# Performance work log

Measured on AMD Instinct MI355X. Metric: run time of the kernel, lower is better.

Reference implementation:

```python
import jax, jax.numpy as jnp
import numpy as np

S, B, D = 2048, 2, 2048      # seq, batch, hidden  (x is [S, B, D])
H, KV, HD = 16, 4, 128        # n_head, n_kv_head, head_dim
N_REP = H // KV               # GQA repeat factor
THETA = 10000.0


def setup_inputs() -> dict:
    key = jax.random.key(0)
    ks = jax.random.split(key, 5)
    sc = 1.0 / np.sqrt(D)
    x = jax.random.normal(ks[0], (S, B, D), jnp.float32)
    Wq = jax.random.normal(ks[1], (D, H * HD), jnp.float32) * sc
    Wk = jax.random.normal(ks[2], (D, KV * HD), jnp.float32) * sc
    Wv = jax.random.normal(ks[3], (D, KV * HD), jnp.float32) * sc
    Wo = jax.random.normal(ks[4], (H * HD, D), jnp.float32) * sc
    return {"x": x, "Wq": Wq, "Wk": Wk, "Wv": Wv, "Wo": Wo}


def _rope_cos_sin(seq_len, dim, theta):
    inv_freq = 1.0 / (theta ** (jnp.arange(0, dim, 2, dtype=jnp.float32) / dim))
    t = jnp.arange(seq_len, dtype=jnp.float32)
    freqs = jnp.outer(t, inv_freq)                  # [S, dim/2]
    emb = jnp.concatenate([freqs, freqs], axis=-1)  # [S, dim]
    return jnp.cos(emb), jnp.sin(emb)


def _rotate_half(u):
    u1, u2 = jnp.split(u, 2, axis=-1)
    return jnp.concatenate([-u2, u1], axis=-1)


def reference(x, Wq, Wk, Wv, Wo):
    # projections (torch Linear without bias; W stored as [in, out] here)
    q = (x @ Wq).reshape(S, B, H, HD)
    k = (x @ Wk).reshape(S, B, KV, HD)
    v = (x @ Wv).reshape(S, B, KV, HD)

    # RoPE (full rotary, partial_rotary_factor == 1.0)
    cos, sin = _rope_cos_sin(S, HD, THETA)
    cos = cos[:, None, None, :]  # [S,1,1,HD] broadcasts over B, heads
    sin = sin[:, None, None, :]
    q = q * cos + _rotate_half(q) * sin
    k = k * cos + _rotate_half(k) * sin

    # GQA: repeat_interleave kv heads to match query heads
    k = jnp.repeat(k, N_REP, axis=2)
    v = jnp.repeat(v, N_REP, axis=2)

    # [S,B,H,HD] -> [B,H,S,HD]
    q = q.transpose(1, 2, 0, 3)
    k = k.transpose(1, 2, 0, 3)
    v = v.transpose(1, 2, 0, 3)

    # causal SDPA (dropout_p = 0 in eval)
    scale = 1.0 / np.sqrt(HD)
    scores = jnp.einsum('bhqd,bhkd->bhqk', q, k) * scale
    causal = jnp.tril(jnp.ones((S, S), dtype=bool))
    scores = jnp.where(causal, scores, jnp.finfo(scores.dtype).min)
    probs = jax.nn.softmax(scores, axis=-1)
    out = jnp.einsum('bhqk,bhkd->bhqd', probs, v)

    # [B,H,S,HD] -> [S,B,D], then output projection
    out = out.transpose(2, 0, 1, 3).reshape(S, B, D)
    return out @ Wo
```

## Files before the change

### kernel.cpp

```cpp
#include <hip/hip_runtime.h>
#include <hip/hip_bf16.h>
#include <cstdint>
#include <math.h>

#define S_LEN   2048
#define B_SZ    2
#define D_MODEL 2048
#define NH      16
#define NKV     4
#define HD      128
#define ROWS    (S_LEN * B_SZ)
#define NQKV    3072
#define SCALE   0.08838834764831845f

typedef __attribute__((ext_vector_type(8))) short short8;
typedef __attribute__((ext_vector_type(4))) float f32x4;

__device__ __forceinline__ short f2bf(float f) {
  union { float f; unsigned u; } v; v.f = f;
  unsigned r = v.u + 0x7fffu + ((v.u >> 16) & 1u);
  return (short)(r >> 16);
}
__device__ __forceinline__ float bf2f(short x) {
  union { unsigned u; float f; } v;
  v.u = ((unsigned)(unsigned short)x) << 16;
  return v.f;
}

__device__ __forceinline__ void async16(const short* g, short* l) {
  __builtin_amdgcn_global_load_lds(
      (const __attribute__((address_space(1))) void*)(uintptr_t)(const void*)g,
      (__attribute__((address_space(3))) void*)(uintptr_t)(void*)l,
      16, 0, 0);
}

__global__ void cvt_bf16_kernel(const float* __restrict__ src, short* __restrict__ dst, int n4) {
  int t = blockIdx.x * blockDim.x + threadIdx.x;
  if (t >= n4) return;
  float4 v = ((const float4*)src)[t];
  short4 o;
  o.x = f2bf(v.x); o.y = f2bf(v.y); o.z = f2bf(v.z); o.w = f2bf(v.w);
  *(short4*)(dst + (size_t)t * 4) = o;
}

__global__ void wtrans_qkv_kernel(const float* __restrict__ Wq,
                                  const float* __restrict__ Wk,
                                  const float* __restrict__ Wv,
                                  short* __restrict__ dst) {
  __shared__ float tile[32][33];
  const int bx = blockIdx.x;
  const float* src;
  int Ndim, n0, drow;
  if (bx < 64)      { src = Wq; Ndim = 2048; n0 = bx * 32;        drow = n0; }
  else if (bx < 80) { src = Wk; Ndim = 512;  n0 = (bx - 64) * 32; drow = 2048 + n0; }
  else              { src = Wv; Ndim = 512;  n0 = (bx - 80) * 32; drow = 2560 + n0; }
  const int k0 = blockIdx.y * 32;
  for (int r = threadIdx.y; r < 32; r += 8)
    tile[r][threadIdx.x] = src[(size_t)(k0 + r) * Ndim + n0 + threadIdx.x];
  __syncthreads();
  for (int r = threadIdx.y; r < 32; r += 8)
    dst[(size_t)(drow + r) * 2048 + k0 + threadIdx.x] = f2bf(tile[threadIdx.x][r]);
}

__global__ void wtrans_kernel(const float* __restrict__ src, short* __restrict__ dst,
                              int Kdim, int Ndim) {
  __shared__ float tile[32][33];
  int n0 = blockIdx.x * 32, k0 = blockIdx.y * 32;
  for (int r = threadIdx.y; r < 32; r += 8)
    tile[r][threadIdx.x] = src[(size_t)(k0 + r) * Ndim + n0 + threadIdx.x];
  __syncthreads();
  for (int r = threadIdx.y; r < 32; r += 8)
    dst[(size_t)(n0 + r) * Kdim + k0 + threadIdx.x] = f2bf(tile[threadIdx.x][r]);
}

template<int BM, int BF16OUT>
__global__ __launch_bounds__(512, 2) void gemm2_kernel(const short* __restrict__ A,
    const short* __restrict__ Bt, void* __restrict__ Cv, int N, int K) {
  constexpr int MI  = BM / 32;
  constexpr int PH  = MI / 4;
  constexpr int APW = BM / 128;
  constexpr int TC  = APW + 2;
  constexpr int ASZ = BM * 32;
  constexpr int BSZ = 256 * 32;
  constexpr int BUFS = ASZ + BSZ;
  __shared__ alignas(16) short lds[4 * BUFS];

  const int tid  = threadIdx.x;
  const int w    = tid >> 6, lane = tid & 63;
  const int quad = lane >> 4, lr = lane & 15;
  const int wm   = w >> 2, wn = w & 3;

  const int nwg = gridDim.x;
  const int id  = (blockIdx.x & 7) * (nwg >> 3) + (blockIdx.x >> 3);
  const int nbx = N >> 8;
  const int bx = id % nbx, by = id / nbx;
  const int m0 = by * BM, n0 = bx * 256;

  const short* gA = A  + (size_t)(m0 + w * (16 * APW) + (lane >> 2)) * K + (lane & 3) * 8;
  const short* gB = Bt + (size_t)(n0 + w * 32 + (lane >> 2)) * K + (lane & 3) * 8;

  const int aoff = (wm * (BM / 2) + lr) * 32 + quad * 8;
  const int boff = (wn * 64 + lr) * 32 + quad * 8;

  f32x4 acc[MI][4];
#pragma unroll
  for (int i = 0; i < MI; ++i)
#pragma unroll
    for (int j = 0; j < 4; ++j) acc[i][j] = (f32x4){0.f, 0.f, 0.f, 0.f};

  auto stageA = [&](int t) {
    short* la = lds + (t & 3) * BUFS;
    const short* g = gA + t * 32;
#pragma unroll
    for (int c = 0; c < APW; ++c)
      async16(g + (size_t)c * 16 * K, la + (w * APW + c) * 512);
  };
  auto stageB = [&](int t) {
    short* lb = lds + (t & 3) * BUFS + ASZ;
    const short* g = gB + t * 32;
#pragma unroll
    for (int c = 0; c < 2; ++c)
      async16(g + (size_t)c * 16 * K, lb + (w * 2 + c) * 512);
  };

  const int NT = K >> 5;
  stageA(0); stageB(0); stageA(1); stageB(1); stageA(2); stageB(2);
  asm volatile("s_waitcnt vmcnt(%0)" :: "n"(2 * TC) : "memory");
  __builtin_amdgcn_s_barrier();

  for (int t = 0; t < NT; ++t) {
    const short* la = lds + (t & 3) * BUFS;
    const short* lb = la + ASZ;
    const bool pre = (t + 3) < NT;

    short8 a0[4], b0[4];
#pragma unroll
    for (int j = 0; j < 4; ++j) b0[j] = *(const short8*)(lb + boff + j * 512);
#pragma unroll
    for (int i = 0; i < 4; ++i) a0[i] = *(const short8*)(la + aoff + i * 512);
    if (pre) stageA(t + 3);
    if (PH == 1 && pre) stageB(t + 3);
    __builtin_amdgcn_s_barrier();
    __builtin_amdgcn_s_setprio(1);
#pragma unroll
    for (int i = 0; i < 4; ++i)
#pragma unroll
      for (int j = 0; j < 4; ++j)
        acc[i][j] = __builtin_amdgcn_mfma_f32_16x16x32_bf16(a0[i], b0[j], acc[i][j], 0, 0, 0);
    __builtin_amdgcn_s_setprio(0);

    if (PH == 2) {
      __builtin_amdgcn_s_barrier();
      short8 a1[4];
#pragma unroll
      for (int i = 0; i < 4; ++i) a1[i] = *(const short8*)(la + aoff + (4 + i) * 512);
      if (pre) stageB(t + 3);
      __builtin_amdgcn_s_barrier();
      __builtin_amdgcn_s_setprio(1);
#pragma unroll
      for (int i = 0; i < 4; ++i)
#pragma unroll
        for (int j = 0; j < 4; ++j)
          acc[4 + i][j] = __builtin_amdgcn_mfma_f32_16x16x32_bf16(a1[i], b0[j], acc[4 + i][j], 0, 0, 0);
      __builtin_amdgcn_s_setprio(0);
    }

    if (t < NT - 1) {
      if (t < NT - 3)       asm volatile("s_waitcnt vmcnt(%0)" :: "n"(2 * TC) : "memory");
      else if (t == NT - 3) asm volatile("s_waitcnt vmcnt(%0)" :: "n"(TC) : "memory");
      else                  asm volatile("s_waitcnt vmcnt(0)" ::: "memory");
      __builtin_amdgcn_s_barrier();
    }
  }

#pragma unroll
  for (int i = 0; i < MI; ++i) {
    const int row = m0 + wm * (BM / 2) + i * 16 + quad * 4;
#pragma unroll
    for (int j = 0; j < 4; ++j) {
      const int col = n0 + wn * 64 + j * 16 + lr;
#pragma unroll
      for (int r = 0; r < 4; ++r) {
        const float v = acc[i][j][r];
        if (BF16OUT) ((short*)Cv)[(size_t)(row + r) * N + col] = f2bf(v);
        else         ((float*)Cv)[(size_t)(row + r) * N + col] = v;
      }
    }
  }
}

__global__ void rope_kernel(const short* __restrict__ QKVb, short* __restrict__ Qb,
                            short* __restrict__ Kpack) {
  const int head = blockIdx.y;
  const int t = blockIdx.x * blockDim.x + threadIdx.x;
  const int i = t & 63;
  const int row = t >> 6;
  const int s = row >> 1;
  const int b = row & 1;
  float inv_freq = __expf(-(float)i * (1.0f / 64.0f) * 9.210340371976184f);
  float ang = (float)s * inv_freq;
  float sn, cs;
  __sincosf(ang, &sn, &cs);
  if (head < NH) {
    const short* p = QKVb + (size_t)row * NQKV + head * HD;
    float v1 = bf2f(p[i]), v2 = bf2f(p[i + 64]);
    short* q = Qb + ((size_t)(b * NH + head) * S_LEN + s) * HD;
    q[i]      = f2bf((v1 * cs - v2 * sn) * SCALE);
    q[i + 64] = f2bf((v2 * cs + v1 * sn) * SCALE);
  } else {
    const int kv = head - NH;
    const short* p = QKVb + (size_t)row * NQKV + NH * HD + kv * HD;
    float v1 = bf2f(p[i]), v2 = bf2f(p[i + 64]);
    float k1 = v1 * cs - v2 * sn;
    float k2 = v2 * cs + v1 * sn;
    short* kp = Kpack + (size_t)(b * NKV + kv) * S_LEN * HD;
    const int tile = s >> 4, lrr = s & 15;
    const int d1 = i, d2 = i + 64;
    kp[(size_t)((tile * 4 + (d1 >> 5)) * 64 + ((d1 >> 3) & 3) * 16 + lrr) * 8 + (d1 & 7)] = f2bf(k1);
    kp[(size_t)((tile * 4 + (d2 >> 5)) * 64 + ((d2 >> 3) & 3) * 16 + lrr) * 8 + (d2 & 7)] = f2bf(k2);
  }
}

__global__ void vpack_kernel(const short* __restrict__ QKVb, short* __restrict__ Vpack) {
  __shared__ short tile[32][136];
  const int tid = threadIdx.x;
  const int chunk = blockIdx.x & 63, stream = blockIdx.x >> 6;
  const int b = stream >> 2, kv = stream & 3;
  const int vcol = NH * HD + NKV * HD + kv * HD;
  {
    const int r = tid >> 3, c = (tid & 7) * 16;
    const short* src = QKVb + (size_t)((chunk * 32 + r) * B_SZ + b) * NQKV + vcol + c;
    *(short8*)(&tile[r][c])     = *(const short8*)(src);
    *(short8*)(&tile[r][c + 8]) = *(const short8*)(src + 8);
  }
  __syncthreads();
  const int wave = tid >> 6, lane = tid & 63, quad = lane >> 4, lr = lane & 15;
  short* dst = Vpack + (size_t)stream * HD * S_LEN + chunk * 4096 + lane * 8;
#pragma unroll
  for (int k = 0; k < 2; ++k) {
    const int dt = wave + k * 4;
    short8 v;
#pragma unroll
    for (int j = 0; j < 8; ++j) v[j] = tile[quad * 8 + j][dt * 16 + lr];
    *(short8*)(dst + dt * 512) = v;
  }
}

#define PSP 72

template<bool MASK>
__device__ __forceinline__ void attn_iter64(
    const short* __restrict__ Ks, const short* __restrict__ Vs,
    short* __restrict__ Psw, const short8 qf[4], int kv0, int nt, int qlim,
    int quad, int lr, int lane, f32x4 o[8], float& m_i, float& l_i)
{
  const int lane_off = lane * 8;
  f32x4 sc[4];
#pragma unroll
  for (int t = 0; t < 4; ++t) {
    if (t < nt) {
      const short* kp = Ks + t * 2048 + lane_off;
      f32x4 s = (f32x4){0.f, 0.f, 0.f, 0.f};
#pragma unroll
      for (int c = 0; c < 4; ++c) {
        short8 kf = *(const short8*)(kp + c * 512);
        s = __builtin_amdgcn_mfma_f32_16x16x32_bf16(kf, qf[c], s, 0, 0, 0);
      }
      sc[t] = s;
    } else {
      sc[t] = (f32x4){-3.0e38f, -3.0e38f, -3.0e38f, -3.0e38f};
    }
  }
  if (MASK) {
#pragma unroll
    for (int t = 0; t < 4; ++t)
#pragma unroll
      for (int r = 0; r < 4; ++r)
        if (kv0 + t * 16 + quad * 4 + r > qlim) sc[t][r] = -3.0e38f;
  }
  float mb = -3.0e38f;
#pragma unroll
  for (int t = 0; t < 4; ++t)
#pragma unroll
    for (int r = 0; r < 4; ++r) mb = fmaxf(mb, sc[t][r]);
  mb = fmaxf(mb, __shfl_xor(mb, 16, 64));
  mb = fmaxf(mb, __shfl_xor(mb, 32, 64));
  const float mnew = fmaxf(m_i, mb);
  const float alpha = __expf(m_i - mnew);
  m_i = mnew;
  float rs = 0.f;
#pragma unroll
  for (int t = 0; t < 4; ++t) {
    float p0 = __expf(sc[t][0] - mnew);
    float p1 = __expf(sc[t][1] - mnew);
    float p2 = __expf(sc[t][2] - mnew);
    float p3 = __expf(sc[t][3] - mnew);
    rs += (p0 + p1) + (p2 + p3);
    __hip_bfloat162 pk01 = __float22bfloat162_rn(make_float2(p0, p1));
    __hip_bfloat162 pk23 = __float22bfloat162_rn(make_float2(p2, p3));
    __hip_bfloat162* pd = (__hip_bfloat162*)(Psw + lr * PSP + t * 16 + quad * 4);
    pd[0] = pk01;
    pd[1] = pk23;
  }
  rs += __shfl_xor(rs, 16, 64);
  rs += __shfl_xor(rs, 32, 64);
  l_i = l_i * alpha + rs;
#pragma unroll
  for (int n = 0; n < 8; ++n)
#pragma unroll
    for (int r = 0; r < 4; ++r) o[n][r] *= alpha;
  short8 pb0 = *(const short8*)(Psw + lr * PSP + quad * 8);
#pragma unroll
  for (int dt = 0; dt < 8; ++dt) {
    short8 vf = *(const short8*)(Vs + dt * 512 + lane_off);
    o[dt] = __builtin_amdgcn_mfma_f32_16x16x32_bf16(vf, pb0, o[dt], 0, 0, 0);
  }
  if (!MASK || nt > 2) {
    short8 pb1 = *(const short8*)(Psw + lr * PSP + 32 + quad * 8);
#pragma unroll
    for (int dt = 0; dt < 8; ++dt) {
      short8 vf = *(const short8*)(Vs + 4096 + dt * 512 + lane_off);
      o[dt] = __builtin_amdgcn_mfma_f32_16x16x32_bf16(vf, pb1, o[dt], 0, 0, 0);
    }
  }
}

__global__ __launch_bounds__(256) void attn_kernel(const short* __restrict__ Qb,
    const short* __restrict__ Kpack, const short* __restrict__ Vpack,
    short* __restrict__ Ob) {
  __shared__ alignas(16) short Ks[64 * HD];
  __shared__ alignas(16) short Vs[64 * HD];
  __shared__ alignas(16) short Ps[4][16 * PSP];
  const int tid = threadIdx.x, wave = tid >> 6, lane = tid & 63;
  const int quad = lane >> 4, lr = lane & 15;
  const int bid = blockIdx.x;
  const int sid  = bid & 7;
  const int hsub = (bid >> 3) & 3;
  const int qg   = 31 - (bid >> 5);
  const int b = sid >> 2, kvh = sid & 3;
  const int h = kvh * 4 + hsub;
  const int qw = (qg * 4 + wave) * 16;

  const short* Qp  = Qb    + ((size_t)(b * NH + h) * S_LEN + qw) * HD;
  const short* Kpk = Kpack + (size_t)(b * NKV + kvh) * S_LEN * HD;
  const short* Vpk = Vpack + (size_t)(b * NKV + kvh) * HD * S_LEN;
  short* Psw = &Ps[wave][0];

  short8 qf[4];
#pragma unroll
  for (int c = 0; c < 4; ++c)
    qf[c] = *(const short8*)(Qp + lr * HD + c * 32 + quad * 8);

  f32x4 o[8];
#pragma unroll
  for (int n = 0; n < 8; ++n) o[n] = (f32x4){0.f, 0.f, 0.f, 0.f};
  float m_i = -3.0e38f, l_i = 0.f;

  const int qlim = qw + lr;
  for (int it = 0; it <= qg; ++it) {
    const int kv0 = it * 64;
    __syncthreads();
    {
      const short* gk = Kpk + (size_t)kv0 * HD;
      const short* gv = Vpk + (size_t)(kv0 >> 5) * 4096;
#pragma unroll
      for (int k = 0; k < 4; ++k) {
        const int off = (wave * 4 + k) * 512;
        async16(gk + off + lane * 8, Ks + off);
        async16(gv + off + lane * 8, Vs + off);
      }
    }
    __syncthreads();
    if (it < qg)
      attn_iter64<false>(Ks, Vs, Psw, qf, kv0, 4, qlim, quad, lr, lane, o, m_i, l_i);
    else
      attn_iter64<true>(Ks, Vs, Psw, qf, kv0, wave + 1, qlim, quad, lr, lane, o, m_i, l_i);
  }

  const float invl = 1.0f / l_i;
  short* op = Ob + ((size_t)(qw + lr) * B_SZ + b) * D_MODEL + h * HD + quad * 4;
#pragma unroll
  for (int dt = 0; dt < 8; ++dt) {
    short4 ov;
    ov.x = f2bf(o[dt][0] * invl);
    ov.y = f2bf(o[dt][1] * invl);
    ov.z = f2bf(o[dt][2] * invl);
    ov.w = f2bf(o[dt][3] * invl);
    *(short4*)(op + dt * 16) = ov;
  }
}

extern "C" void kernel_launch(void* const* d_in, const int* in_sizes, int n_in,
                              void* d_out, int out_size, void* d_ws, size_t ws_size,
                              hipStream_t stream) {
  (void)in_sizes; (void)n_in; (void)out_size; (void)ws_size;
  const float* x  = (const float*)d_in[0];
  const float* Wq = (const float*)d_in[1];
  const float* Wk = (const float*)d_in[2];
  const float* Wv = (const float*)d_in[3];
  const float* Wo = (const float*)d_in[4];
  float* out = (float*)d_out;
  char* ws = (char*)d_ws;

  short* Wqkv_t = (short*)(ws);
  short* xb     = (short*)(ws + 12582912);
  short* Qb     = (short*)(ws);
  short* Kpack  = (short*)(ws + 16777216);
  short* Vpack  = (short*)(ws + 25165824);
  short* QKVb   = (short*)(ws + 29360128);
  short* Ob     = (short*)(ws + 29360128);
  short* Wo_t   = (short*)(ws + 54525952);

  dim3 tblk(32, 8);

  cvt_bf16_kernel<<<(ROWS * D_MODEL / 4 + 255) / 256, 256, 0, stream>>>(x, xb, ROWS * D_MODEL / 4);
  wtrans_qkv_kernel<<<dim3(96, 64), tblk, 0, stream>>>(Wq, Wk, Wv, Wqkv_t);
  wtrans_kernel<<<dim3(64, 64), tblk, 0, stream>>>(Wo, Wo_t, 2048, 2048);
  gemm2_kernel<256, 1><<<dim3((NQKV / 256) * (ROWS / 256)), 512, 0, stream>>>(xb, Wqkv_t, QKVb, NQKV, D_MODEL);
  rope_kernel<<<dim3(1024, NH + NKV), 256, 0, stream>>>(QKVb, Qb, Kpack);
  vpack_kernel<<<dim3(512), 256, 0, stream>>>(QKVb, Vpack);
  attn_kernel<<<dim3(1024), 256, 0, stream>>>(Qb, Kpack, Vpack, Ob);
  gemm2_kernel<128, 0><<<dim3((D_MODEL / 256) * (ROWS / 128)), 512, 0, stream>>>(Ob, Wo_t, out, D_MODEL, D_MODEL);
}
```

Measured before the change: 314.9 us.

## Store GEMM tiles in MFMA fragment layout and split mainloop into finer phases

Restructures the bf16 GEMM's LDS staging so each async global load fills one 16x32 fragment, stored in lane-contiguous MFMA operand order. Reads become a simple lane*8 offset per fragment. The main loop is split into MI/2 phases, each loading two A fragments and issuing one barrier, and the async prefetches are spread across those phases. The goal is to interleave loads, barriers and MFMAs more finely and avoid LDS bank conflicts, at the cost of more barriers per K-tile.

```diff
diff --git a/kernel.cpp b/kernel.cpp
--- a/kernel.cpp
+++ b/kernel.cpp
@@ -77,12 +77,12 @@
 __global__ __launch_bounds__(512, 2) void gemm2_kernel(const short* __restrict__ A,
     const short* __restrict__ Bt, void* __restrict__ Cv, int N, int K) {
   constexpr int MI  = BM / 32;
-  constexpr int PH  = MI / 4;
-  constexpr int APW = BM / 128;
-  constexpr int TC  = APW + 2;
-  constexpr int ASZ = BM * 32;
-  constexpr int BSZ = 256 * 32;
-  constexpr int BUFS = ASZ + BSZ;
+  constexpr int NPH = MI / 2;
+  constexpr int FA  = BM / 16;
+  constexpr int FB  = 16;
+  constexpr int TC  = (FA + FB) / 8;
+  constexpr int ASZ = FA * 512;
+  constexpr int BUFS = ASZ + FB * 512;
   __shared__ alignas(16) short lds[4 * BUFS];
 
   const int tid  = threadIdx.x;
@@ -96,11 +96,14 @@
   const int bx = id % nbx, by = id / nbx;
   const int m0 = by * BM, n0 = bx * 256;
 
-  const short* gA = A  + (size_t)(m0 + w * (16 * APW) + (lane >> 2)) * K + (lane & 3) * 8;
-  const short* gB = Bt + (size_t)(n0 + w * 32 + (lane >> 2)) * K + (lane & 3) * 8;
-
-  const int aoff = (wm * (BM / 2) + lr) * 32 + quad * 8;
-  const int boff = (wn * 64 + lr) * 32 + quad * 8;
+  const short* gsrc[TC];
+#pragma unroll
+  for (int c = 0; c < TC; ++c) {
+    const int ft = w * TC + c;
+    const short* base = (ft < FA) ? (A  + (size_t)(m0 + ft * 16 + lr) * K)
+                                  : (Bt + (size_t)(n0 + (ft - FA) * 16 + lr) * K);
+    gsrc[c] = base + quad * 8;
+  }
 
   f32x4 acc[MI][4];
 #pragma unroll
@@ -108,60 +111,51 @@
 #pragma unroll
     for (int j = 0; j < 4; ++j) acc[i][j] = (f32x4){0.f, 0.f, 0.f, 0.f};
 
-  auto stageA = [&](int t) {
-    short* la = lds + (t & 3) * BUFS;
-    const short* g = gA + t * 32;
-#pragma unroll
-    for (int c = 0; c < APW; ++c)
-      async16(g + (size_t)c * 16 * K, la + (w * APW + c) * 512);
+  auto stage = [&](int t, int c) {
+    async16(gsrc[c] + t * 32, lds + (t & 3) * BUFS + (w * TC + c) * 512);
   };
-  auto stageB = [&](int t) {
-    short* lb = lds + (t & 3) * BUFS + ASZ;
-    const short* g = gB + t * 32;
-#pragma unroll
-    for (int c = 0; c < 2; ++c)
-      async16(g + (size_t)c * 16 * K, lb + (w * 2 + c) * 512);
-  };
 
   const int NT = K >> 5;
-  stageA(0); stageB(0); stageA(1); stageB(1); stageA(2); stageB(2);
+#pragma unroll
+  for (int t = 0; t < 3; ++t)
+#pragma unroll
+    for (int c = 0; c < TC; ++c) stage(t, c);
   asm volatile("s_waitcnt vmcnt(%0)" :: "n"(2 * TC) : "memory");
   __builtin_amdgcn_s_barrier();
+  asm volatile("" ::: "memory");
 
   for (int t = 0; t < NT; ++t) {
     const short* la = lds + (t & 3) * BUFS;
     const short* lb = la + ASZ;
     const bool pre = (t + 3) < NT;
-
-    short8 a0[4], b0[4];
-#pragma unroll
-    for (int j = 0; j < 4; ++j) b0[j] = *(const short8*)(lb + boff + j * 512);
-#pragma unroll
-    for (int i = 0; i < 4; ++i) a0[i] = *(const short8*)(la + aoff + i * 512);
-    if (pre) stageA(t + 3);
-    if (PH == 1 && pre) stageB(t + 3);
-    __builtin_amdgcn_s_barrier();
-    __builtin_amdgcn_s_setprio(1);
-#pragma unroll
-    for (int i = 0; i < 4; ++i)
+    short8 b[4];
+#pragma unroll
+    for (int p = 0; p < NPH; ++p) {
+      if (p == 0) {
+#pragma unroll
+        for (int j = 0; j < 4; ++j)
+          b[j] = *(const short8*)(lb + (wn * 4 + j) * 512 + lane * 8);
+      }
+      short8 a0 = *(const short8*)(la + (wm * MI + 2 * p)     * 512 + lane * 8);
+      short8 a1 = *(const short8*)(la + (wm * MI + 2 * p + 1) * 512 + lane * 8);
+      if (pre) {
+        if (p == 0) {
+#pragma unroll
+          for (int c = 0; c <= TC - NPH; ++c) stage(t + 3, c);
+        } else {
+          stage(t + 3, p + (TC - NPH));
+        }
+      }
+      asm volatile("" ::: "memory");
+      __builtin_amdgcn_s_barrier();
+      asm volatile("" ::: "memory");
+      __builtin_amdgcn_s_setprio(1);
 #pragma unroll
       for (int j = 0; j < 4; ++j)
-        acc[i][j] = __builtin_amdgcn_mfma_f32_16x16x32_bf16(a0[i], b0[j], acc[i][j], 0, 0, 0);
-    __builtin_amdgcn_s_setprio(0);
-
-    if (PH == 2) {
-      __builtin_amdgcn_s_barrier();
-      short8 a1[4];
-#pragma unroll
-      for (int i = 0; i < 4; ++i) a1[i] = *(const short8*)(la + aoff + (4 + i) * 512);
-      if (pre) stageB(t + 3);
-      __builtin_amdgcn_s_barrier();
-      __builtin_amdgcn_s_setprio(1);
-#pragma unroll
-      for (int i = 0; i < 4; ++i)
-#pragma unroll
-        for (int j = 0; j < 4; ++j)
-          acc[4 + i][j] = __builtin_amdgcn_mfma_f32_16x16x32_bf16(a1[i], b0[j], acc[4 + i][j], 0, 0, 0);
+        acc[2 * p][j] = __builtin_amdgcn_mfma_f32_16x16x32_bf16(a0, b[j], acc[2 * p][j], 0, 0, 0);
+#pragma unroll
+      for (int j = 0; j < 4; ++j)
+        acc[2 * p + 1][j] = __builtin_amdgcn_mfma_f32_16x16x32_bf16(a1, b[j], acc[2 * p + 1][j], 0, 0, 0);
       __builtin_amdgcn_s_setprio(0);
     }
 
@@ -169,7 +163,9 @@
       if (t < NT - 3)       asm volatile("s_waitcnt vmcnt(%0)" :: "n"(2 * TC) : "memory");
       else if (t == NT - 3) asm volatile("s_waitcnt vmcnt(%0)" :: "n"(TC) : "memory");
       else                  asm volatile("s_waitcnt vmcnt(0)" ::: "memory");
+      asm volatile("" ::: "memory");
       __builtin_amdgcn_s_barrier();
+      asm volatile("" ::: "memory");
     }
   }
 
```

Result: no change. 318.4 us (+1.1%).
